# Kernel optimization log

Measured on AMD Instinct MI355X. Metric: run time of the kernel, lower is better.

The kernel has to match this reference:

```python
import jax, jax.numpy as jnp
import numpy as np

B = 256
NUM_IN_CAPS = 1152   # 6*6*32
NUM_OUT_CAPS = 10
VEC_IN = 8
VEC_OUT = 16
ROUTING_ITERS = 3


def squash(x, axis):
    # squash(v) = |v|^2/(1+|v|^2) * v/|v|  (matches torch module, no eps)
    mag_squ = jnp.sum(x * x, axis=axis, keepdims=True)
    return mag_squ / (1.0 + mag_squ) * (x / jnp.sqrt(mag_squ))


def setup_inputs() -> dict:
    key = jax.random.key(0)
    k = jax.random.split(key, 6)
    x = jax.random.normal(k[0], (B, 1, 28, 28), dtype=jnp.float32)
    conv1_w = jax.random.normal(k[1], (256, 1, 9, 9), dtype=jnp.float32) * 0.1
    conv1_b = jnp.zeros((256,), dtype=jnp.float32)
    pc_w = jax.random.normal(k[2], (256, 256, 9, 9), dtype=jnp.float32) * 0.02  # out = 32 caps * 8 dims
    pc_b = jnp.zeros((256,), dtype=jnp.float32)
    # routing transform W: original shape [1,1152,160,8,1] -> [1152,10,16,8]
    W = jax.random.normal(k[3], (NUM_IN_CAPS, NUM_OUT_CAPS, VEC_OUT, VEC_IN), dtype=jnp.float32)
    dc_bias = jnp.zeros((NUM_OUT_CAPS, VEC_OUT), dtype=jnp.float32)
    return {"x": x, "conv1_w": conv1_w, "conv1_b": conv1_b,
            "pc_w": pc_w, "pc_b": pc_b, "W": W, "dc_bias": dc_bias}


def _conv(x, w, b, stride):
    y = jax.lax.conv_general_dilated(x, w, (stride, stride), 'VALID',
                                     dimension_numbers=('NCHW', 'OIHW', 'NCHW'))
    return y + b[None, :, None, None]


def reference(x, conv1_w, conv1_b, pc_w, pc_b, W, dc_bias):
    # conv1: [B,1,28,28] -> [B,256,20,20]  (no activation in original module)
    h = _conv(x, conv1_w, conv1_b, stride=1)
    # primaryCaps conv: -> [B,256,6,6] -> [B,1152,8]
    caps = _conv(h, pc_w, pc_b, stride=2)
    caps = caps.reshape(caps.shape[0], -1, VEC_IN)          # [B,1152,8]
    caps = squash(caps, axis=-1)
    # u_hat[b,i,j,d] = sum_k W[i,j,d,k] * caps[b,i,k]  (the original broadcast-mul-sum)
    u_hat = jnp.einsum('ijdk,bik->bijd', W, caps)           # [B,1152,10,16]
    b_ij = jnp.zeros(u_hat.shape[:3], dtype=u_hat.dtype)    # [B,1152,10]
    for r in range(ROUTING_ITERS):
        c_ij = jax.nn.softmax(b_ij, axis=2)                 # softmax over output caps
        s_j = jnp.einsum('bij,bijd->bjd', c_ij, u_hat) + dc_bias  # [B,10,16]
        v_j = squash(s_j, axis=-1)
        if r != ROUTING_ITERS - 1:
            b_ij = b_ij + jnp.einsum('bijd,bjd->bij', u_hat, v_j)
    return v_j  # [B,10,16]
```

## Files before the change

kernel.cpp:

```cpp
#include <hip/hip_runtime.h>
#include <hip/hip_bf16.h>


typedef __attribute__((ext_vector_type(8))) short short8;
typedef __attribute__((ext_vector_type(4))) float float4v;

__device__ inline float bfu(ushort v){ return __uint_as_float((unsigned)v << 16); }

__global__ __launch_bounds__(640) void conv1_kernel(const float* __restrict__ x,
    const float* __restrict__ w, const float* __restrict__ bias,
    __hip_bfloat16* __restrict__ ht){
  __shared__ float img[784];
  __shared__ float wsv[32 * 81];
  __shared__ ushort tile[400 * 33];
  int b = blockIdx.x;
  int og = blockIdx.y;
  int t = threadIdx.x;
  const float* xb = x + (size_t)b * 784;
  for (int idx = t; idx < 784; idx += 640) img[idx] = xb[idx];
  for (int idx = t; idx < 2592; idx += 640) wsv[idx] = w[(size_t)og * 2592 + idx];
  __syncthreads();
  int o_l = t / 20;
  int y   = t - o_l * 20;
  float acc[20];
  #pragma unroll
  for (int i = 0; i < 20; i++) acc[i] = 0.f;
  #pragma unroll
  for (int r = 0; r < 9; r++){
    float row[28];
    const float4* rp = (const float4*)&img[(y + r) * 28];
    #pragma unroll
    for (int q = 0; q < 7; q++){
      float4 v4 = rp[q];
      row[4*q+0]=v4.x; row[4*q+1]=v4.y; row[4*q+2]=v4.z; row[4*q+3]=v4.w;
    }
    #pragma unroll
    for (int s = 0; s < 9; s++){
      float wv = wsv[o_l * 81 + r * 9 + s];
      #pragma unroll
      for (int xx = 0; xx < 20; xx++)
        acc[xx] = fmaf(wv, row[xx + s], acc[xx]);
    }
  }
  float bv = bias[og * 32 + o_l];
  #pragma unroll
  for (int xx = 0; xx < 20; xx++){
    __hip_bfloat16 hv = __float2bfloat16(acc[xx] + bv);
    tile[(y * 20 + xx) * 33 + o_l] = *(ushort*)&hv;
  }
  __syncthreads();
  __hip_bfloat16* hb = ht + (size_t)b * 102400 + og * 32;
  for (int idx = t; idx < 6400; idx += 640){
    int pos = idx >> 4, op = idx & 15;
    unsigned v = (unsigned)tile[pos * 33 + op * 2]
               | ((unsigned)tile[pos * 33 + op * 2 + 1] << 16);
    *(unsigned*)(hb + (size_t)pos * 256 + op * 2) = v;
  }
}

__global__ __launch_bounds__(256) void arepack_kernel(const float* __restrict__ w2,
    ushort* __restrict__ A2s){
  __shared__ float wbuf[64 * 81];
  int o = blockIdx.x;
  int t = threadIdx.x;
  int ow = o >> 6, fo = (o >> 4) & 3, l15 = o & 15;
  size_t obase8 = (size_t)ow * 165888 + (size_t)fo * 64 + (size_t)l15 * 4;
  for (int c0 = 0; c0 < 256; c0 += 64){
    __syncthreads();
    for (int idx = t; idx < 5184; idx += 256)
      wbuf[idx] = w2[(size_t)o * 20736 + (size_t)c0 * 81 + idx];
    __syncthreads();
    for (int idx = t; idx < 2592; idx += 256){
      int rs = idx >> 5;
      int cp = (idx & 31) * 2;
      int cg = c0 + cp;
      int ct = cg >> 5, quad = (cg >> 3) & 3, e = cg & 7;
      __hip_bfloat16 b0 = __float2bfloat16(wbuf[cp * 81 + rs]);
      __hip_bfloat16 b1 = __float2bfloat16(wbuf[(cp + 1) * 81 + rs]);
      unsigned pack = (unsigned)*(ushort*)&b0 | ((unsigned)*(ushort*)&b1 << 16);
      size_t si = (obase8 + (size_t)ct * 256 + (size_t)rs * 2048 + quad) * 8 + e;
      *(unsigned*)(A2s + si) = pack;
    }
  }
}

__global__ __launch_bounds__(256) void wrepack_kernel(const float* __restrict__ W,
    ushort* __restrict__ Wrb){
  __shared__ float tile[64][65];
  int r0 = blockIdx.x * 64;
  int c0 = blockIdx.y * 64;
  int t = threadIdx.x; int lx = t & 63, ly = t >> 6;
  for (int rr = ly; rr < 64; rr += 4)
    tile[rr][lx] = W[(size_t)(r0 + rr) * 1280 + c0 + lx];
  __syncthreads();
  for (int rr = ly; rr < 64; rr += 4){
    __hip_bfloat16 hv = __float2bfloat16(tile[lx][rr]);
    Wrb[(size_t)(c0 + rr) * 1152 + r0 + lx] = *(ushort*)&hv;
  }
}

__global__ __launch_bounds__(256, 2) void conv2_mfma_kernel(
    const __hip_bfloat16* __restrict__ ht, const short8* __restrict__ A2,
    float* __restrict__ caps4){
  __shared__ ushort img[2][400 * 40];
  int bx  = blockIdx.x;
  int xcd = bx & 7;
  int kq  = xcd >> 1;
  int p   = ((bx >> 3) << 1) | (xcd & 1);
  int b0  = p * 2;
  int t = threadIdx.x;
  int lane = t & 63;
  int wid  = t >> 6;
  int l15  = lane & 15;
  int quad = lane >> 4;

  int bn[3], slc[3];
  #pragma unroll
  for (int fn = 0; fn < 3; fn++){
    int n = fn * 16 + l15;
    int y = n / 6, xx = n - y * 6;
    if (n >= 36){ y = 0; xx = 0; }
    bn[fn]  = 40 * y + 2 * xx;
    slc[fn] = (quad + 4 * y) % 5;
  }
  const short8* i0p = (const short8*)&img[0][0];
  const short8* i1p = (const short8*)&img[1][0];

  float4v acc[4][6];
  #pragma unroll
  for (int fo = 0; fo < 4; fo++)
    #pragma unroll
    for (int fn = 0; fn < 6; fn++)
      acc[fo][fn] = (float4v){0.f, 0.f, 0.f, 0.f};

  for (int ci = 0; ci < 2; ci++){
    int ct = kq * 2 + ci;
    __syncthreads();
    #pragma unroll
    for (int im = 0; im < 2; im++){
      const __hip_bfloat16* hb = ht + (size_t)(b0 + im) * 102400;
      for (int idx = t; idx < 1600; idx += 256){
        int pp = idx >> 2, q = idx & 3;
        int sl = (q + 2 * (pp / 20)) % 5;
        uint4 v = *(const uint4*)(hb + (size_t)pp * 256 + ct * 32 + q * 8);
        *(uint4*)&img[im][pp * 40 + sl * 8] = v;
      }
    }
    __syncthreads();

    const short8* ap = A2 + ((size_t)wid * 648 + ct) * 256 + l15 * 4 + quad;

    short8 aF[2][4], bF[2][6];
    #pragma unroll
    for (int fo = 0; fo < 4; fo++) aF[0][fo] = ap[fo * 64];
    #pragma unroll
    for (int fn = 0; fn < 6; fn++){
      int f3 = (fn < 3) ? fn : fn - 3;
      const short8* ib = (fn < 3) ? i0p : i1p;
      bF[0][fn] = ib[bn[f3] * 5 + slc[f3]];
    }

    int rn = 0, sn = 0, r2m = 0;
    #pragma unroll 2
    for (int rs = 0; rs < 81; rs++){
      int cur = rs & 1, nxt = cur ^ 1;
      sn++;
      if (sn == 9){ sn = 0; rn++; r2m += 2; if (r2m >= 5) r2m -= 5; }
      int nrs = (rs < 80) ? rs + 1 : 80;
      int roff = rn * 20 + sn;
      const short8* apn = ap + (size_t)nrs * 2048;
      #pragma unroll
      for (int fo = 0; fo < 4; fo++) aF[nxt][fo] = apn[fo * 64];
      #pragma unroll
      for (int fn = 0; fn < 6; fn++){
        int f3 = (fn < 3) ? fn : fn - 3;
        const short8* ib = (fn < 3) ? i0p : i1p;
        int sl = slc[f3] + r2m; if (sl >= 5) sl -= 5;
        bF[nxt][fn] = ib[(bn[f3] + roff) * 5 + sl];
      }
      #pragma unroll
      for (int fo = 0; fo < 4; fo++)
        #pragma unroll
        for (int fn = 0; fn < 6; fn++)
          acc[fo][fn] = __builtin_amdgcn_mfma_f32_16x16x32_bf16(aF[cur][fo], bF[cur][fn], acc[fo][fn], 0, 0, 0);
    }
  }

  #pragma unroll
  for (int fn = 0; fn < 6; fn++){
    int im = (fn < 3) ? 0 : 1;
    int f3 = (fn < 3) ? fn : fn - 3;
    int pos = f3 * 16 + l15;
    if (pos < 36){
      float* cb = caps4 + ((size_t)kq * 256 + b0 + im) * 9216;
      #pragma unroll
      for (int fo = 0; fo < 4; fo++){
        int ob = wid * 64 + fo * 16 + quad * 4;
        #pragma unroll
        for (int rr = 0; rr < 4; rr++)
          cb[(size_t)(ob + rr) * 36 + pos] = acc[fo][fn][rr];
      }
    }
  }
}

__global__ __launch_bounds__(256) void squash4_kernel(const float* __restrict__ caps4,
    const float* __restrict__ bias, float* __restrict__ caps){
  size_t cid = (size_t)blockIdx.x * 256 + threadIdx.x;
  size_t base = cid * 8;
  const size_t STR = 2359296;
  float4 a0 = *(const float4*)(caps4 + base);
  float4 a1 = *(const float4*)(caps4 + base + 4);
  #pragma unroll
  for (int k = 1; k < 4; k++){
    float4 q0 = *(const float4*)(caps4 + k * STR + base);
    float4 q1 = *(const float4*)(caps4 + k * STR + base + 4);
    a0.x+=q0.x; a0.y+=q0.y; a0.z+=q0.z; a0.w+=q0.w;
    a1.x+=q1.x; a1.y+=q1.y; a1.z+=q1.z; a1.w+=q1.w;
  }
  int off = (int)(base % 9216);
  float v[8] = {a0.x,a0.y,a0.z,a0.w,a1.x,a1.y,a1.z,a1.w};
  #pragma unroll
  for (int e = 0; e < 8; e++) v[e] += bias[(off + e) / 36];
  float msq = 0.f;
  #pragma unroll
  for (int e = 0; e < 8; e++) msq += v[e]*v[e];
  float scale = sqrtf(msq) / (1.f + msq);
  float* cp = caps + base;
  #pragma unroll
  for (int e = 0; e < 8; e++) cp[e] = v[e]*scale;
}

__global__ __launch_bounds__(256) void uhat_t_kernel(const float* __restrict__ caps,
    const ushort* __restrict__ Wrb, ushort* __restrict__ uT){
  __shared__ float cl[8 * 16 * 64];
  int i0  = blockIdx.x * 64;
  int by  = blockIdx.y;
  int b0  = (by >> 2) * 16;
  int jd0 = (by & 3) * 40;
  int t = threadIdx.x, lane = t & 63, w = t >> 6;
  for (int f = t; f < 2048; f += 256){
    int base = f * 4; int bb = base >> 9; int r = base & 511;
    int il = r >> 3; int k = r & 7;
    float4 v = *(const float4*)(caps + ((size_t)(b0+bb)*1152 + i0 + il)*8 + k);
    cl[((k+0)*16+bb)*64+il] = v.x;
    cl[((k+1)*16+bb)*64+il] = v.y;
    cl[((k+2)*16+bb)*64+il] = v.z;
    cl[((k+3)*16+bb)*64+il] = v.w;
  }
  __syncthreads();
  for (int jj = 0; jj < 10; jj++){
    int jd = jd0 + w * 10 + jj;
    float wk[8];
    #pragma unroll
    for (int k = 0; k < 8; k++)
      wk[k] = bfu(Wrb[((size_t)jd * 8 + k) * 1152 + i0 + lane]);
    #pragma unroll
    for (int bb = 0; bb < 16; bb++){
      float acc = 0.f;
      #pragma unroll
      for (int k = 0; k < 8; k++) acc = fmaf(wk[k], cl[(k*16+bb)*64+lane], acc);
      __hip_bfloat16 hv = __float2bfloat16(acc);
      uT[((size_t)(b0+bb)*160 + jd)*1152 + i0 + lane] = *(ushort*)&hv;
    }
  }
}

__global__ __launch_bounds__(384) void routeAB_kernel(
    const ushort* __restrict__ uT, const float* __restrict__ vin,
    float* __restrict__ bbuf, float* __restrict__ spart, int mode){
  __shared__ float c_l[384 * 11];
  __shared__ float vs[160];
  int ic = blockIdx.x;
  int b  = blockIdx.y;
  int t = threadIdx.x;
  int lane = t & 63, w = t >> 6;
  const ushort* ub = uT + (size_t)b * 184320 + ic * 384;

  if (mode){
    if (t < 160) vs[t] = vin[b * 160 + t];
    __syncthreads();
    const ushort* up = ub + t;
    float d[10];
    #pragma unroll
    for (int j = 0; j < 10; j++){
      float dj = 0.f;
      #pragma unroll
      for (int dd = 0; dd < 16; dd++){
        int jd = j * 16 + dd;
        dj = fmaf(bfu(up[(size_t)jd * 1152]), vs[jd], dj);
      }
      d[j] = dj;
    }
    float* bp = bbuf + ((size_t)b * 1152 + ic * 384 + t) * 10;
    if (mode == 2){
      #pragma unroll
      for (int j = 0; j < 10; j++) d[j] += bp[j];
    } else {
      #pragma unroll
      for (int j = 0; j < 10; j++) bp[j] = d[j];
    }
    float m = d[0];
    #pragma unroll
    for (int j = 1; j < 10; j++) m = fmaxf(m, d[j]);
    float se = 0.f;
    #pragma unroll
    for (int j = 0; j < 10; j++){ d[j] = __expf(d[j] - m); se += d[j]; }
    float inv = 1.f / se;
    #pragma unroll
    for (int j = 0; j < 10; j++) c_l[t * 11 + j] = d[j] * inv;
  }
  __syncthreads();

  for (int jd = w; jd < 160; jd += 6){
    const uint* urow32 = (const uint*)(ub + (size_t)jd * 1152);
    float sacc = 0.f;
    if (mode){
      int jj = jd >> 4;
      #pragma unroll
      for (int st = 0; st < 3; st++){
        uint uv = urow32[st * 64 + lane];
        int i_l = (st * 64 + lane) * 2;
        sacc = fmaf(bfu((ushort)(uv & 0xffffu)), c_l[i_l * 11 + jj], sacc);
        sacc = fmaf(bfu((ushort)(uv >> 16)),     c_l[(i_l + 1) * 11 + jj], sacc);
      }
    } else {
      #pragma unroll
      for (int st = 0; st < 3; st++){
        uint uv = urow32[st * 64 + lane];
        sacc += bfu((ushort)(uv & 0xffffu)) + bfu((ushort)(uv >> 16));
      }
    }
    sacc += __shfl_xor(sacc, 32);
    sacc += __shfl_xor(sacc, 16);
    sacc += __shfl_xor(sacc, 8);
    sacc += __shfl_xor(sacc, 4);
    sacc += __shfl_xor(sacc, 2);
    sacc += __shfl_xor(sacc, 1);
    if (lane == 0) spart[((size_t)ic * 256 + b) * 160 + jd] = mode ? sacc : sacc * 0.1f;
  }
}

__global__ __launch_bounds__(160) void vsq_kernel(const float* __restrict__ spart,
    const float* __restrict__ dcb, float* __restrict__ vout){
  int b = blockIdx.x;
  int t = threadIdx.x;
  float s = dcb[t];
  #pragma unroll
  for (int ic = 0; ic < 3; ic++) s += spart[((size_t)ic * 256 + b) * 160 + t];
  float msq = s * s;
  msq += __shfl_xor(msq, 1, 16);
  msq += __shfl_xor(msq, 2, 16);
  msq += __shfl_xor(msq, 4, 16);
  msq += __shfl_xor(msq, 8, 16);
  float scale = sqrtf(msq) / (1.f + msq);
  vout[b * 160 + t] = s * scale;
}

extern "C" void kernel_launch(void* const* d_in, const int* in_sizes, int n_in,
                              void* d_out, int out_size, void* d_ws, size_t ws_size,
                              hipStream_t stream){
  (void)in_sizes; (void)n_in; (void)out_size; (void)ws_size;
  const float* x   = (const float*)d_in[0];
  const float* w1  = (const float*)d_in[1];
  const float* b1  = (const float*)d_in[2];
  const float* w2  = (const float*)d_in[3];
  const float* b2  = (const float*)d_in[4];
  const float* W   = (const float*)d_in[5];
  const float* dcb = (const float*)d_in[6];
  float* out = (float*)d_out;

  char* ws = (char*)d_ws;
  __hip_bfloat16* ht = (__hip_bfloat16*)(ws);
  ushort* A2s  = (ushort*)(ws + 52428800);
  float* caps4 = (float*)(ws + 63045632);
  ushort* uT   = (ushort*)(ws);
  float* caps  = (float*)(ws + 100794368);
  ushort* Wrb  = (ushort*)(ws + 110231552);
  float* bbuf  = (float*)(ws + 113180672);
  float* spart = (float*)(ws + 124977152);
  float* vbuf  = (float*)(ws + 125468672);

  conv1_kernel<<<dim3(256, 8), 640, 0, stream>>>(x, w1, b1, ht);
  arepack_kernel<<<256, 256, 0, stream>>>(w2, A2s);
  wrepack_kernel<<<dim3(18, 20), 256, 0, stream>>>(W, Wrb);
  conv2_mfma_kernel<<<512, 256, 0, stream>>>(ht, (const short8*)A2s, caps4);
  squash4_kernel<<<1152, 256, 0, stream>>>(caps4, b2, caps);
  uhat_t_kernel<<<dim3(18, 64), 256, 0, stream>>>(caps, Wrb, uT);
  routeAB_kernel<<<dim3(3, 256), 384, 0, stream>>>(uT, vbuf, bbuf, spart, 0);
  vsq_kernel<<<256, 160, 0, stream>>>(spart, dcb, vbuf);
  routeAB_kernel<<<dim3(3, 256), 384, 0, stream>>>(uT, vbuf, bbuf, spart, 1);
  vsq_kernel<<<256, 160, 0, stream>>>(spart, dcb, vbuf);
  routeAB_kernel<<<dim3(3, 256), 384, 0, stream>>>(uT, vbuf, bbuf, spart, 2);
  vsq_kernel<<<256, 160, 0, stream>>>(spart, dcb, out);
}
```

Measured before the change: 407.2 us.

## Process one image per conv2 block to halve LDS and accumulators

The conv2 MFMA kernel now handles one image per block instead of two, so it launches 1024 blocks, allocates half the LDS and half the accumulator registers, and raises the launch-bounds occupancy hint from 2 to 3. The LDS B-fragment addressing is replaced with incrementally updated byte offsets, and the A pointer is advanced incrementally, to cut index arithmetic. The aim is more resident waves and less address math. In exchange, each A-weight fragment loaded from global memory now feeds only one image, doubling weight traffic and halving MFMA reuse per A load. The XCD-aware block mapping is also dropped.

Measured after the change: 698.6 us. 71.6% more time.

```diff
diff --git a/kernel.cpp b/kernel.cpp
--- a/kernel.cpp
+++ b/kernel.cpp
@@ -99,15 +99,13 @@
   }
 }
 
-__global__ __launch_bounds__(256, 2) void conv2_mfma_kernel(
+__global__ __launch_bounds__(256, 3) void conv2_mfma_kernel(
     const __hip_bfloat16* __restrict__ ht, const short8* __restrict__ A2,
     float* __restrict__ caps4){
-  __shared__ ushort img[2][400 * 40];
-  int bx  = blockIdx.x;
-  int xcd = bx & 7;
-  int kq  = xcd >> 1;
-  int p   = ((bx >> 3) << 1) | (xcd & 1);
-  int b0  = p * 2;
+  __shared__ ushort img[400 * 40];
+  int bx = blockIdx.x;
+  int b  = bx & 255;
+  int kq = bx >> 8;
   int t = threadIdx.x;
   int lane = t & 63;
   int wid  = t >> 6;
@@ -123,76 +121,78 @@
     bn[fn]  = 40 * y + 2 * xx;
     slc[fn] = (quad + 4 * y) % 5;
   }
-  const short8* i0p = (const short8*)&img[0][0];
-  const short8* i1p = (const short8*)&img[1][0];
-
-  float4v acc[4][6];
+  const char* ibase = (const char*)&img[0];
+
+  float4v acc[4][3];
   #pragma unroll
   for (int fo = 0; fo < 4; fo++)
     #pragma unroll
-    for (int fn = 0; fn < 6; fn++)
+    for (int fn = 0; fn < 3; fn++)
       acc[fo][fn] = (float4v){0.f, 0.f, 0.f, 0.f};
+
+  const __hip_bfloat16* hb = ht + (size_t)b * 102400;
 
   for (int ci = 0; ci < 2; ci++){
     int ct = kq * 2 + ci;
     __syncthreads();
-    #pragma unroll
-    for (int im = 0; im < 2; im++){
-      const __hip_bfloat16* hb = ht + (size_t)(b0 + im) * 102400;
-      for (int idx = t; idx < 1600; idx += 256){
-        int pp = idx >> 2, q = idx & 3;
-        int sl = (q + 2 * (pp / 20)) % 5;
-        uint4 v = *(const uint4*)(hb + (size_t)pp * 256 + ct * 32 + q * 8);
-        *(uint4*)&img[im][pp * 40 + sl * 8] = v;
-      }
-    }
-    __syncthreads();
-
-    const short8* ap = A2 + ((size_t)wid * 648 + ct) * 256 + l15 * 4 + quad;
-
-    short8 aF[2][4], bF[2][6];
-    #pragma unroll
-    for (int fo = 0; fo < 4; fo++) aF[0][fo] = ap[fo * 64];
-    #pragma unroll
-    for (int fn = 0; fn < 6; fn++){
-      int f3 = (fn < 3) ? fn : fn - 3;
-      const short8* ib = (fn < 3) ? i0p : i1p;
-      bF[0][fn] = ib[bn[f3] * 5 + slc[f3]];
-    }
-
-    int rn = 0, sn = 0, r2m = 0;
+    for (int idx = t; idx < 1600; idx += 256){
+      int pp = idx >> 2, q = idx & 3;
+      int sl = (q + 2 * (pp / 20)) % 5;
+      uint4 v = *(const uint4*)(hb + (size_t)pp * 256 + ct * 32 + q * 8);
+      *(uint4*)&img[pp * 40 + sl * 8] = v;
+    }
+    __syncthreads();
+
+    const char* apb = (const char*)(A2 + ((size_t)wid * 648 + ct) * 256 + l15 * 4 + quad);
+
+    int boff[3], bsl[3];
+    #pragma unroll
+    for (int fn = 0; fn < 3; fn++){
+      bsl[fn]  = slc[fn];
+      boff[fn] = bn[fn] * 80 + slc[fn] * 16;
+    }
+
+    short8 aF[2][4], bF[2][3];
+    #pragma unroll
+    for (int fo = 0; fo < 4; fo++) aF[0][fo] = *(const short8*)(apb + fo * 1024);
+    #pragma unroll
+    for (int fn = 0; fn < 3; fn++) bF[0][fn] = *(const short8*)(ibase + boff[fn]);
+
+    int sn = 0;
     #pragma unroll 2
     for (int rs = 0; rs < 81; rs++){
       int cur = rs & 1, nxt = cur ^ 1;
       sn++;
-      if (sn == 9){ sn = 0; rn++; r2m += 2; if (r2m >= 5) r2m -= 5; }
-      int nrs = (rs < 80) ? rs + 1 : 80;
-      int roff = rn * 20 + sn;
-      const short8* apn = ap + (size_t)nrs * 2048;
-      #pragma unroll
-      for (int fo = 0; fo < 4; fo++) aF[nxt][fo] = apn[fo * 64];
-      #pragma unroll
-      for (int fn = 0; fn < 6; fn++){
-        int f3 = (fn < 3) ? fn : fn - 3;
-        const short8* ib = (fn < 3) ? i0p : i1p;
-        int sl = slc[f3] + r2m; if (sl >= 5) sl -= 5;
-        bF[nxt][fn] = ib[(bn[f3] + roff) * 5 + sl];
-      }
+      if (sn == 9){
+        sn = 0;
+        #pragma unroll
+        for (int fn = 0; fn < 3; fn++){
+          bsl[fn] += 2;
+          if (bsl[fn] >= 5){ bsl[fn] -= 5; boff[fn] += 912; }
+          else             {               boff[fn] += 992; }
+        }
+      } else {
+        #pragma unroll
+        for (int fn = 0; fn < 3; fn++) boff[fn] += 80;
+      }
+      apb += (rs < 80) ? 32768 : 0;
+      #pragma unroll
+      for (int fo = 0; fo < 4; fo++) aF[nxt][fo] = *(const short8*)(apb + fo * 1024);
+      #pragma unroll
+      for (int fn = 0; fn < 3; fn++) bF[nxt][fn] = *(const short8*)(ibase + boff[fn]);
       #pragma unroll
       for (int fo = 0; fo < 4; fo++)
         #pragma unroll
-        for (int fn = 0; fn < 6; fn++)
+        for (int fn = 0; fn < 3; fn++)
           acc[fo][fn] = __builtin_amdgcn_mfma_f32_16x16x32_bf16(aF[cur][fo], bF[cur][fn], acc[fo][fn], 0, 0, 0);
     }
   }
 
   #pragma unroll
-  for (int fn = 0; fn < 6; fn++){
-    int im = (fn < 3) ? 0 : 1;
-    int f3 = (fn < 3) ? fn : fn - 3;
-    int pos = f3 * 16 + l15;
+  for (int fn = 0; fn < 3; fn++){
+    int pos = fn * 16 + l15;
     if (pos < 36){
-      float* cb = caps4 + ((size_t)kq * 256 + b0 + im) * 9216;
+      float* cb = caps4 + ((size_t)kq * 256 + b) * 9216;
       #pragma unroll
       for (int fo = 0; fo < 4; fo++){
         int ob = wid * 64 + fo * 16 + quad * 4;
@@ -384,7 +384,7 @@
   conv1_kernel<<<dim3(256, 8), 640, 0, stream>>>(x, w1, b1, ht);
   arepack_kernel<<<256, 256, 0, stream>>>(w2, A2s);
   wrepack_kernel<<<dim3(18, 20), 256, 0, stream>>>(W, Wrb);
-  conv2_mfma_kernel<<<512, 256, 0, stream>>>(ht, (const short8*)A2s, caps4);
+  conv2_mfma_kernel<<<1024, 256, 0, stream>>>(ht, (const short8*)A2s, caps4);
   squash4_kernel<<<1152, 256, 0, stream>>>(caps4, b2, caps);
   uhat_t_kernel<<<dim3(18, 64), 256, 0, stream>>>(caps, Wrb, uT);
   routeAB_kernel<<<dim3(3, 256), 384, 0, stream>>>(uT, vbuf, bbuf, spart, 0);
```

## Fuse first routing iteration's weighted sum into the u_hat kernel

Applied to the files above, without the earlier changes.

In the first routing iteration every coupling coefficient is a uniform 0.1, so s_j is just 0.1 times the sum of u_hat over input capsules. The u_hat kernel now reduces each computed value across the wavefront and writes per-chunk partial sums into a buffer that shares space with bbuf. A new vsq18 kernel sums the 18 chunks, applies the scale and bias, and squashes. This drops one full routeAB pass over the large bf16 u_hat tensor, at the cost of extra shuffle reductions and small scattered writes inside the u_hat kernel.

After: 435.9 us. 1.07x slower.

```diff
diff --git a/kernel.cpp b/kernel.cpp
--- a/kernel.cpp
+++ b/kernel.cpp
@@ -232,9 +232,11 @@
 }
 
 __global__ __launch_bounds__(256) void uhat_t_kernel(const float* __restrict__ caps,
-    const ushort* __restrict__ Wrb, ushort* __restrict__ uT){
+    const ushort* __restrict__ Wrb, ushort* __restrict__ uT,
+    float* __restrict__ spart18){
   __shared__ float cl[8 * 16 * 64];
-  int i0  = blockIdx.x * 64;
+  int ichunk = blockIdx.x;
+  int i0  = ichunk * 64;
   int by  = blockIdx.y;
   int b0  = (by >> 2) * 16;
   int jd0 = (by & 3) * 40;
@@ -262,6 +264,15 @@
       for (int k = 0; k < 8; k++) acc = fmaf(wk[k], cl[(k*16+bb)*64+lane], acc);
       __hip_bfloat16 hv = __float2bfloat16(acc);
       uT[((size_t)(b0+bb)*160 + jd)*1152 + i0 + lane] = *(ushort*)&hv;
+      float sacc = acc;
+      sacc += __shfl_xor(sacc, 32);
+      sacc += __shfl_xor(sacc, 16);
+      sacc += __shfl_xor(sacc, 8);
+      sacc += __shfl_xor(sacc, 4);
+      sacc += __shfl_xor(sacc, 2);
+      sacc += __shfl_xor(sacc, 1);
+      if (lane == 0)
+        spart18[((size_t)ichunk * 256 + b0 + bb) * 160 + jd] = sacc;
     }
   }
 }
@@ -348,6 +359,23 @@
   float s = dcb[t];
   #pragma unroll
   for (int ic = 0; ic < 3; ic++) s += spart[((size_t)ic * 256 + b) * 160 + t];
+  float msq = s * s;
+  msq += __shfl_xor(msq, 1, 16);
+  msq += __shfl_xor(msq, 2, 16);
+  msq += __shfl_xor(msq, 4, 16);
+  msq += __shfl_xor(msq, 8, 16);
+  float scale = sqrtf(msq) / (1.f + msq);
+  vout[b * 160 + t] = s * scale;
+}
+
+__global__ __launch_bounds__(160) void vsq18_kernel(const float* __restrict__ spart18,
+    const float* __restrict__ dcb, float* __restrict__ vout){
+  int b = blockIdx.x;
+  int t = threadIdx.x;
+  float s = 0.f;
+  #pragma unroll
+  for (int c = 0; c < 18; c++) s += spart18[((size_t)c * 256 + b) * 160 + t];
+  s = dcb[t] + 0.1f * s;
   float msq = s * s;
   msq += __shfl_xor(msq, 1, 16);
   msq += __shfl_xor(msq, 2, 16);
@@ -378,6 +406,7 @@
   float* caps  = (float*)(ws + 100794368);
   ushort* Wrb  = (ushort*)(ws + 110231552);
   float* bbuf  = (float*)(ws + 113180672);
+  float* spart18 = (float*)(ws + 113180672);
   float* spart = (float*)(ws + 124977152);
   float* vbuf  = (float*)(ws + 125468672);
 
@@ -386,9 +415,8 @@
   wrepack_kernel<<<dim3(18, 20), 256, 0, stream>>>(W, Wrb);
   conv2_mfma_kernel<<<512, 256, 0, stream>>>(ht, (const short8*)A2s, caps4);
   squash4_kernel<<<1152, 256, 0, stream>>>(caps4, b2, caps);
-  uhat_t_kernel<<<dim3(18, 64), 256, 0, stream>>>(caps, Wrb, uT);
-  routeAB_kernel<<<dim3(3, 256), 384, 0, stream>>>(uT, vbuf, bbuf, spart, 0);
-  vsq_kernel<<<256, 160, 0, stream>>>(spart, dcb, vbuf);
+  uhat_t_kernel<<<dim3(18, 64), 256, 0, stream>>>(caps, Wrb, uT, spart18);
+  vsq18_kernel<<<256, 160, 0, stream>>>(spart18, dcb, vbuf);
   routeAB_kernel<<<dim3(3, 256), 384, 0, stream>>>(uT, vbuf, bbuf, spart, 1);
   vsq_kernel<<<256, 160, 0, stream>>>(spart, dcb, vbuf);
   routeAB_kernel<<<dim3(3, 256), 384, 0, stream>>>(uT, vbuf, bbuf, spart, 2);
```

## Fuse u_hat recompute into routing and track cumulative v instead of logits

Applied to the files above, without the earlier changes.

Drops the materialised bf16 u_hat tensor (B×160×1152) and the stored routing logits. Each routing pass recomputes u_hat on the fly from W and caps, with W staged through double-buffered shared memory. It uses the identity that b_ij equals u_hat dotted with the running sum of v_j, so only that cumulative v is kept per batch. The softmax uses an online max/sum over a first pass, followed by a second pass that accumulates s_j. This removes large global writes and reads of u_hat and the logits, at the cost of recomputing the W·caps products two to three times per iteration and an 18-way partial-sum reduction.

New measurement: 602.7 us. 48.0% more time.

```diff
diff --git a/kernel.cpp b/kernel.cpp
--- a/kernel.cpp
+++ b/kernel.cpp
@@ -84,18 +84,26 @@
   }
 }
 
-__global__ __launch_bounds__(256) void wrepack_kernel(const float* __restrict__ W,
-    ushort* __restrict__ Wrb){
-  __shared__ float tile[64][65];
-  int r0 = blockIdx.x * 64;
-  int c0 = blockIdx.y * 64;
-  int t = threadIdx.x; int lx = t & 63, ly = t >> 6;
-  for (int rr = ly; rr < 64; rr += 4)
-    tile[rr][lx] = W[(size_t)(r0 + rr) * 1280 + c0 + lx];
-  __syncthreads();
-  for (int rr = ly; rr < 64; rr += 4){
-    __hip_bfloat16 hv = __float2bfloat16(tile[lx][rr]);
-    Wrb[(size_t)(c0 + rr) * 1152 + r0 + lx] = *(ushort*)&hv;
+__global__ __launch_bounds__(256) void wrepack2_kernel(const float* __restrict__ W,
+    ushort* __restrict__ Wrb2){
+  int ic = blockIdx.x;
+  int j  = blockIdx.y;
+  int t = threadIdx.x;
+  for (int it = t; it < 1024; it += 256){
+    int d = it >> 6, il = it & 63;
+    const float* src = W + (size_t)(ic*64 + il)*1280 + j*128 + d*8;
+    float4 a = *(const float4*)src;
+    float4 b = *(const float4*)(src + 4);
+    float vals[8] = {a.x,a.y,a.z,a.w,b.x,b.y,b.z,b.w};
+    unsigned p[4];
+    #pragma unroll
+    for (int e = 0; e < 4; e++){
+      __hip_bfloat16 h0 = __float2bfloat16(vals[2*e]);
+      __hip_bfloat16 h1 = __float2bfloat16(vals[2*e+1]);
+      p[e] = (unsigned)*(ushort*)&h0 | ((unsigned)*(ushort*)&h1 << 16);
+    }
+    uint4 pv = {p[0], p[1], p[2], p[3]};
+    *(uint4*)(Wrb2 + ((((size_t)ic*10 + j)*16 + d)*64 + il)*8) = pv;
   }
 }
 
@@ -231,130 +239,161 @@
   for (int e = 0; e < 8; e++) cp[e] = v[e]*scale;
 }
 
-__global__ __launch_bounds__(256) void uhat_t_kernel(const float* __restrict__ caps,
-    const ushort* __restrict__ Wrb, ushort* __restrict__ uT){
-  __shared__ float cl[8 * 16 * 64];
-  int i0  = blockIdx.x * 64;
-  int by  = blockIdx.y;
-  int b0  = (by >> 2) * 16;
-  int jd0 = (by & 3) * 40;
-  int t = threadIdx.x, lane = t & 63, w = t >> 6;
-  for (int f = t; f < 2048; f += 256){
+__global__ __launch_bounds__(256) void route_fused_kernel(
+    const float* __restrict__ caps, const ushort* __restrict__ Wrb2,
+    const float* __restrict__ vsum, float* __restrict__ spart, int mode){
+  __shared__ float cl[8 * 8 * 64];
+  __shared__ ushort Wt[2][16 * 64 * 8];
+  __shared__ float vsl[8 * 160];
+  int ic = blockIdx.x;
+  int b0 = blockIdx.y * 8;
+  int t = threadIdx.x, lane = t & 63, wid = t >> 6;
+  int bbA = wid * 2, bbB = bbA + 1;
+
+  for (int f = t; f < 1024; f += 256){
     int base = f * 4; int bb = base >> 9; int r = base & 511;
     int il = r >> 3; int k = r & 7;
-    float4 v = *(const float4*)(caps + ((size_t)(b0+bb)*1152 + i0 + il)*8 + k);
-    cl[((k+0)*16+bb)*64+il] = v.x;
-    cl[((k+1)*16+bb)*64+il] = v.y;
-    cl[((k+2)*16+bb)*64+il] = v.z;
-    cl[((k+3)*16+bb)*64+il] = v.w;
-  }
+    float4 v = *(const float4*)(caps + ((size_t)(b0+bb)*1152 + ic*64 + il)*8 + k);
+    cl[((k+0)*8+bb)*64+il] = v.x;
+    cl[((k+1)*8+bb)*64+il] = v.y;
+    cl[((k+2)*8+bb)*64+il] = v.z;
+    cl[((k+3)*8+bb)*64+il] = v.w;
+  }
+  if (mode)
+    for (int f = t; f < 1280; f += 256) vsl[f] = vsum[(size_t)b0 * 160 + f];
   __syncthreads();
-  for (int jj = 0; jj < 10; jj++){
-    int jd = jd0 + w * 10 + jj;
-    float wk[8];
-    #pragma unroll
-    for (int k = 0; k < 8; k++)
-      wk[k] = bfu(Wrb[((size_t)jd * 8 + k) * 1152 + i0 + lane]);
-    #pragma unroll
-    for (int bb = 0; bb < 16; bb++){
-      float acc = 0.f;
-      #pragma unroll
-      for (int k = 0; k < 8; k++) acc = fmaf(wk[k], cl[(k*16+bb)*64+lane], acc);
-      __hip_bfloat16 hv = __float2bfloat16(acc);
-      uT[((size_t)(b0+bb)*160 + jd)*1152 + i0 + lane] = *(ushort*)&hv;
-    }
-  }
-}
-
-__global__ __launch_bounds__(384) void routeAB_kernel(
-    const ushort* __restrict__ uT, const float* __restrict__ vin,
-    float* __restrict__ bbuf, float* __restrict__ spart, int mode){
-  __shared__ float c_l[384 * 11];
-  __shared__ float vs[160];
-  int ic = blockIdx.x;
-  int b  = blockIdx.y;
-  int t = threadIdx.x;
-  int lane = t & 63, w = t >> 6;
-  const ushort* ub = uT + (size_t)b * 184320 + ic * 384;
+
+  float clrA[8], clrB[8];
+  #pragma unroll
+  for (int k = 0; k < 8; k++){
+    clrA[k] = cl[(k*8 + bbA)*64 + lane];
+    clrB[k] = cl[(k*8 + bbB)*64 + lane];
+  }
+
+  const uint4* wsrc = (const uint4*)(Wrb2 + (size_t)ic * 81920);
+  uint4* wd0 = (uint4*)&Wt[0][0];
+  uint4* wd1 = (uint4*)&Wt[1][0];
+
+  float m0 = -1e30f, m1 = -1e30f, z0 = 0.f, z1 = 0.f;
 
   if (mode){
-    if (t < 160) vs[t] = vin[b * 160 + t];
-    __syncthreads();
-    const ushort* up = ub + t;
-    float d[10];
-    #pragma unroll
-    for (int j = 0; j < 10; j++){
-      float dj = 0.f;
-      #pragma unroll
-      for (int dd = 0; dd < 16; dd++){
-        int jd = j * 16 + dd;
-        dj = fmaf(bfu(up[(size_t)jd * 1152]), vs[jd], dj);
-      }
-      d[j] = dj;
-    }
-    float* bp = bbuf + ((size_t)b * 1152 + ic * 384 + t) * 10;
-    if (mode == 2){
-      #pragma unroll
-      for (int j = 0; j < 10; j++) d[j] += bp[j];
-    } else {
-      #pragma unroll
-      for (int j = 0; j < 10; j++) bp[j] = d[j];
-    }
-    float m = d[0];
-    #pragma unroll
-    for (int j = 1; j < 10; j++) m = fmaxf(m, d[j]);
-    float se = 0.f;
-    #pragma unroll
-    for (int j = 0; j < 10; j++){ d[j] = __expf(d[j] - m); se += d[j]; }
-    float inv = 1.f / se;
-    #pragma unroll
-    for (int j = 0; j < 10; j++) c_l[t * 11 + j] = d[j] * inv;
-  }
+    #pragma unroll
+    for (int u = 0; u < 4; u++) wd0[t + 256*u] = wsrc[t + 256*u];
+    __syncthreads();
+    for (int jg = 0; jg < 10; jg++){
+      if (jg < 9){
+        uint4* wd = (jg & 1) ? wd0 : wd1;
+        const uint4* wsp = wsrc + (size_t)(jg+1) * 1024;
+        #pragma unroll
+        for (int u = 0; u < 4; u++) wd[t + 256*u] = wsp[t + 256*u];
+      }
+      const ushort* wb = (jg & 1) ? &Wt[1][0] : &Wt[0][0];
+      float da = 0.f, db = 0.f;
+      #pragma unroll
+      for (int jdl = 0; jdl < 16; jdl++){
+        uint4 wv = *(const uint4*)&wb[((size_t)jdl*64 + lane)*8];
+        float wk[8];
+        wk[0]=bfu((ushort)(wv.x&0xffffu)); wk[1]=bfu((ushort)(wv.x>>16));
+        wk[2]=bfu((ushort)(wv.y&0xffffu)); wk[3]=bfu((ushort)(wv.y>>16));
+        wk[4]=bfu((ushort)(wv.z&0xffffu)); wk[5]=bfu((ushort)(wv.z>>16));
+        wk[6]=bfu((ushort)(wv.w&0xffffu)); wk[7]=bfu((ushort)(wv.w>>16));
+        float u0 = 0.f, u1 = 0.f;
+        #pragma unroll
+        for (int k = 0; k < 8; k++){
+          u0 = fmaf(wk[k], clrA[k], u0);
+          u1 = fmaf(wk[k], clrB[k], u1);
+        }
+        int jd = jg*16 + jdl;
+        da = fmaf(u0, vsl[bbA*160 + jd], da);
+        db = fmaf(u1, vsl[bbB*160 + jd], db);
+      }
+      float n0 = fmaxf(m0, da);
+      z0 = z0 * __expf(m0 - n0) + __expf(da - n0);
+      m0 = n0;
+      float n1 = fmaxf(m1, db);
+      z1 = z1 * __expf(m1 - n1) + __expf(db - n1);
+      m1 = n1;
+      __syncthreads();
+    }
+  }
+  float iz0 = mode ? 1.f / z0 : 0.f;
+  float iz1 = mode ? 1.f / z1 : 0.f;
+
+  #pragma unroll
+  for (int u = 0; u < 4; u++) wd0[t + 256*u] = wsrc[t + 256*u];
   __syncthreads();
-
-  for (int jd = w; jd < 160; jd += 6){
-    const uint* urow32 = (const uint*)(ub + (size_t)jd * 1152);
-    float sacc = 0.f;
-    if (mode){
-      int jj = jd >> 4;
-      #pragma unroll
-      for (int st = 0; st < 3; st++){
-        uint uv = urow32[st * 64 + lane];
-        int i_l = (st * 64 + lane) * 2;
-        sacc = fmaf(bfu((ushort)(uv & 0xffffu)), c_l[i_l * 11 + jj], sacc);
-        sacc = fmaf(bfu((ushort)(uv >> 16)),     c_l[(i_l + 1) * 11 + jj], sacc);
-      }
-    } else {
-      #pragma unroll
-      for (int st = 0; st < 3; st++){
-        uint uv = urow32[st * 64 + lane];
-        sacc += bfu((ushort)(uv & 0xffffu)) + bfu((ushort)(uv >> 16));
-      }
-    }
-    sacc += __shfl_xor(sacc, 32);
-    sacc += __shfl_xor(sacc, 16);
-    sacc += __shfl_xor(sacc, 8);
-    sacc += __shfl_xor(sacc, 4);
-    sacc += __shfl_xor(sacc, 2);
-    sacc += __shfl_xor(sacc, 1);
-    if (lane == 0) spart[((size_t)ic * 256 + b) * 160 + jd] = mode ? sacc : sacc * 0.1f;
-  }
-}
-
-__global__ __launch_bounds__(160) void vsq_kernel(const float* __restrict__ spart,
-    const float* __restrict__ dcb, float* __restrict__ vout){
+  for (int jg = 0; jg < 10; jg++){
+    if (jg < 9){
+      uint4* wd = (jg & 1) ? wd0 : wd1;
+      const uint4* wsp = wsrc + (size_t)(jg+1) * 1024;
+      #pragma unroll
+      for (int u = 0; u < 4; u++) wd[t + 256*u] = wsp[t + 256*u];
+    }
+    const ushort* wb = (jg & 1) ? &Wt[1][0] : &Wt[0][0];
+    float u0[16], u1[16];
+    float da = 0.f, db = 0.f;
+    #pragma unroll
+    for (int jdl = 0; jdl < 16; jdl++){
+      uint4 wv = *(const uint4*)&wb[((size_t)jdl*64 + lane)*8];
+      float wk[8];
+      wk[0]=bfu((ushort)(wv.x&0xffffu)); wk[1]=bfu((ushort)(wv.x>>16));
+      wk[2]=bfu((ushort)(wv.y&0xffffu)); wk[3]=bfu((ushort)(wv.y>>16));
+      wk[4]=bfu((ushort)(wv.z&0xffffu)); wk[5]=bfu((ushort)(wv.z>>16));
+      wk[6]=bfu((ushort)(wv.w&0xffffu)); wk[7]=bfu((ushort)(wv.w>>16));
+      float a0 = 0.f, a1 = 0.f;
+      #pragma unroll
+      for (int k = 0; k < 8; k++){
+        a0 = fmaf(wk[k], clrA[k], a0);
+        a1 = fmaf(wk[k], clrB[k], a1);
+      }
+      u0[jdl] = a0; u1[jdl] = a1;
+      if (mode){
+        int jd = jg*16 + jdl;
+        da = fmaf(a0, vsl[bbA*160 + jd], da);
+        db = fmaf(a1, vsl[bbB*160 + jd], db);
+      }
+    }
+    float cv0 = mode ? __expf(da - m0) * iz0 : 0.1f;
+    float cv1 = mode ? __expf(db - m1) * iz1 : 0.1f;
+    float r0 = 0.f, r1 = 0.f;
+    #pragma unroll
+    for (int jdl = 0; jdl < 16; jdl++){
+      float t0 = cv0 * u0[jdl];
+      float t1 = cv1 * u1[jdl];
+      t0 += __shfl_xor(t0, 32); t1 += __shfl_xor(t1, 32);
+      t0 += __shfl_xor(t0, 16); t1 += __shfl_xor(t1, 16);
+      t0 += __shfl_xor(t0, 8);  t1 += __shfl_xor(t1, 8);
+      t0 += __shfl_xor(t0, 4);  t1 += __shfl_xor(t1, 4);
+      t0 += __shfl_xor(t0, 2);  t1 += __shfl_xor(t1, 2);
+      t0 += __shfl_xor(t0, 1);  t1 += __shfl_xor(t1, 1);
+      if (lane == jdl){ r0 = t0; r1 = t1; }
+    }
+    if (lane < 16){
+      spart[((size_t)ic*256 + b0 + bbA)*160 + jg*16 + lane] = r0;
+      spart[((size_t)ic*256 + b0 + bbB)*160 + jg*16 + lane] = r1;
+    }
+    __syncthreads();
+  }
+}
+
+__global__ __launch_bounds__(160) void vsqF_kernel(const float* __restrict__ spart,
+    const float* __restrict__ dcb, float* __restrict__ vsum,
+    float* __restrict__ out, int mode){
   int b = blockIdx.x;
   int t = threadIdx.x;
   float s = dcb[t];
   #pragma unroll
-  for (int ic = 0; ic < 3; ic++) s += spart[((size_t)ic * 256 + b) * 160 + t];
+  for (int c = 0; c < 18; c++) s += spart[((size_t)c * 256 + b) * 160 + t];
   float msq = s * s;
   msq += __shfl_xor(msq, 1, 16);
   msq += __shfl_xor(msq, 2, 16);
   msq += __shfl_xor(msq, 4, 16);
   msq += __shfl_xor(msq, 8, 16);
   float scale = sqrtf(msq) / (1.f + msq);
-  vout[b * 160 + t] = s * scale;
+  float v = s * scale;
+  if (mode == 2)      out[b * 160 + t] = v;
+  else if (mode == 1) vsum[b * 160 + t] += v;
+  else                vsum[b * 160 + t] = v;
 }
 
 extern "C" void kernel_launch(void* const* d_in, const int* in_sizes, int n_in,
@@ -374,23 +413,21 @@
   __hip_bfloat16* ht = (__hip_bfloat16*)(ws);
   ushort* A2s  = (ushort*)(ws + 52428800);
   float* caps4 = (float*)(ws + 63045632);
-  ushort* uT   = (ushort*)(ws);
   float* caps  = (float*)(ws + 100794368);
-  ushort* Wrb  = (ushort*)(ws + 110231552);
-  float* bbuf  = (float*)(ws + 113180672);
-  float* spart = (float*)(ws + 124977152);
-  float* vbuf  = (float*)(ws + 125468672);
+  ushort* Wrb2 = (ushort*)(ws + 110231552);
+  float* spart = (float*)(ws + 113180672);
+  float* vsum  = (float*)(ws + 116129792);
 
   conv1_kernel<<<dim3(256, 8), 640, 0, stream>>>(x, w1, b1, ht);
   arepack_kernel<<<256, 256, 0, stream>>>(w2, A2s);
-  wrepack_kernel<<<dim3(18, 20), 256, 0, stream>>>(W, Wrb);
+  wrepack2_kernel<<<dim3(18, 10), 256, 0, stream>>>(W, Wrb2);
   conv2_mfma_kernel<<<512, 256, 0, stream>>>(ht, (const short8*)A2s, caps4);
   squash4_kernel<<<1152, 256, 0, stream>>>(caps4, b2, caps);
-  uhat_t_kernel<<<dim3(18, 64), 256, 0, stream>>>(caps, Wrb, uT);
-  routeAB_kernel<<<dim3(3, 256), 384, 0, stream>>>(uT, vbuf, bbuf, spart, 0);
-  vsq_kernel<<<256, 160, 0, stream>>>(spart, dcb, vbuf);
-  routeAB_kernel<<<dim3(3, 256), 384, 0, stream>>>(uT, vbuf, bbuf, spart, 1);
-  vsq_kernel<<<256, 160, 0, stream>>>(spart, dcb, vbuf);
-  routeAB_kernel<<<dim3(3, 256), 384, 0, stream>>>(uT, vbuf, bbuf, spart, 2);
-  vsq_kernel<<<256, 160, 0, stream>>>(spart, dcb, out);
-}
+
+  route_fused_kernel<<<dim3(18, 32), 256, 0, stream>>>(caps, Wrb2, vsum, spart, 0);
+  vsqF_kernel<<<256, 160, 0, stream>>>(spart, dcb, vsum, out, 0);
+  route_fused_kernel<<<dim3(18, 32), 256, 0, stream>>>(caps, Wrb2, vsum, spart, 1);
+  vsqF_kernel<<<256, 160, 0, stream>>>(spart, dcb, vsum, out, 1);
+  route_fused_kernel<<<dim3(18, 32), 256, 0, stream>>>(caps, Wrb2, vsum, spart, 2);
+  vsqF_kernel<<<256, 160, 0, stream>>>(spart, dcb, vsum, out, 2);
+}
```
